# Kernel tuning notes

Hardware: AMD Instinct MI355X
Metric: run time of the kernel (lower is better)

The kernel has to match this reference:

```python
import jax, jax.numpy as jnp
import numpy as np

A_NUM = 9
C_NUM = 20


def generate_anchor(anc, grid):
    # anc: (A,2) w,h ; grid: (B,H,W,2) centers -> anchors (B,A,H,W,4)
    centers = grid[:, None]                      # (B,1,H,W,2)
    half = anc.reshape(1, -1, 1, 1, 2) * 0.5     # (1,A,1,1,2)
    return jnp.concatenate([centers - half, centers + half], axis=-1)


def iou_matrix(proposals, bboxes):
    # proposals: (B,A,H,W,4) -> (B,K,4); bboxes: (B,N,5)
    B = proposals.shape[0]
    p = proposals.reshape(B, -1, 4)[:, :, None, :]   # (B,K,1,4)
    bb = bboxes[:, None, :, :]                       # (B,1,N,5)
    s_p = (p[..., 2] - p[..., 0]) * (p[..., 3] - p[..., 1])
    s_b = (bb[..., 2] - bb[..., 0]) * (bb[..., 3] - bb[..., 1])
    ix1 = jnp.maximum(p[..., 0], bb[..., 0])
    iy1 = jnp.maximum(p[..., 1], bb[..., 1])
    ix2 = jnp.minimum(p[..., 2], bb[..., 2])
    iy2 = jnp.minimum(p[..., 3], bb[..., 3])
    s_i = jnp.clip(ix2 - ix1, 0.0) * jnp.clip(iy2 - iy1, 0.0)
    s_u = s_p + s_b - s_i
    iou = jnp.clip(s_i / (s_u + 1e-8), 0.0)
    invalid = (s_u <= 0) | (s_p <= 0) | (s_b <= 0) | (bb[..., 0] < 0)
    return jnp.where(invalid, 0.0, iou)              # (B,K,N)


def extract_anchor_data(anchor_data, idx):
    # anchor_data: (B,A,D,H,W) -> flat (B*A*H*W, D) -> gather
    B, A, D, H, W = anchor_data.shape
    flat = jnp.transpose(anchor_data, (0, 1, 3, 4, 2)).reshape(-1, D)
    return flat[idx]


def extract_class_scores(all_scores, idx, num_anchors):
    # all_scores: (B,C,H,W) -> (B,A,H,W,C) flat -> gather
    B, C, H, W = all_scores.shape
    s = jnp.transpose(all_scores, (0, 2, 3, 1))[:, None]          # (B,1,H,W,C)
    s = jnp.broadcast_to(s, (B, num_anchors, H, W, C)).reshape(-1, C)
    return s[idx]


def setup_inputs() -> dict:
    key = jax.random.key(0)
    ks = jax.random.split(key, 8)
    B, Cin, H, W = 32, 1280, 28, 28
    N, M = 64, 4096
    hid, out_ch = 128, 5 * A_NUM + C_NUM
    features = jax.random.normal(ks[0], (B, Cin, H, W), dtype=jnp.float32)
    # grid of feature-cell centers (GenerateGrid-style)
    xs = jnp.arange(W, dtype=jnp.float32) + 0.5
    ys = jnp.arange(H, dtype=jnp.float32) + 0.5
    gx, gy = jnp.meshgrid(xs, ys, indexing='xy')
    grid = jnp.broadcast_to(jnp.stack([gx, gy], axis=-1), (B, H, W, 2))
    anc = jnp.array([[1.0, 1], [2, 2], [3, 3], [4, 4], [5, 5], [2, 3], [3, 2], [3, 5], [5, 3]], dtype=jnp.float32)
    tl = jax.random.uniform(ks[1], (B, N, 2), minval=0.0, maxval=20.0)
    wh = jax.random.uniform(ks[2], (B, N, 2), minval=1.0, maxval=8.0)
    cls = jax.random.randint(ks[3], (B, N, 1), 0, C_NUM).astype(jnp.float32)
    bb = jnp.concatenate([tl, tl + wh, cls], axis=-1)
    valid = jax.random.uniform(ks[4], (B, N, 1)) > 0.25
    bboxes = jnp.where(valid, bb, -1.0)
    K = B * A_NUM * H * W
    pos_anchor_idx = jax.random.randint(ks[5], (M,), 0, K, dtype=jnp.int64 if jax.config.jax_enable_x64 else jnp.int32)
    neg_anchor_idx = jax.random.randint(ks[6], (M,), 0, K, dtype=pos_anchor_idx.dtype)
    W1 = jax.random.normal(ks[7], (hid, Cin), dtype=jnp.float32) * 0.02
    b1 = jnp.zeros((hid,), dtype=jnp.float32)
    W2 = jax.random.normal(jax.random.fold_in(key, 99), (out_ch, hid), dtype=jnp.float32) * 0.02
    b2 = jnp.zeros((out_ch,), dtype=jnp.float32)
    return {"features": features, "grid": grid, "anc": anc, "bboxes": bboxes,
            "pos_anchor_idx": pos_anchor_idx, "neg_anchor_idx": neg_anchor_idx,
            "W1": W1, "b1": b1, "W2": W2, "b2": b2}


def reference(features, grid, anc, bboxes, pos_anchor_idx, neg_anchor_idx, W1, b1, W2, b2):
    B, Cin, H, W = features.shape
    A, C = A_NUM, C_NUM
    # anchors + broadcast IoU matrix
    anchors = generate_anchor(anc, grid)                 # (B,A,H,W,4)
    iou_mat = iou_matrix(anchors, bboxes)                # (B,A*H*W,N)
    # prediction head: 1x1 conv -> (dropout eval: identity) -> leaky_relu -> 1x1 conv
    h = jnp.einsum('bchw,oc->bohw', features, W1) + b1[None, :, None, None]
    h = jax.nn.leaky_relu(h, negative_slope=0.01)
    out = jnp.einsum('bchw,oc->bohw', h, W2) + b2[None, :, None, None]  # (B,5A+C,H,W)
    anchor_raw = out[:, :5 * A].reshape(B, A, 5, H, W)
    conf_sq = jax.nn.sigmoid(anchor_raw[:, :, 0:1])      # (B,A,1,H,W)
    off_raw = anchor_raw[:, :, 1:]                       # (B,A,4,H,W)
    off_sq = jnp.concatenate([jax.nn.sigmoid(off_raw[:, :, :2]) - 0.5, off_raw[:, :, 2:]], axis=2)
    class_raw = out[:, 5 * A:]                           # (B,C,H,W)
    # training path: irregular gathers
    class_scores = extract_class_scores(class_raw, pos_anchor_idx, A)   # (M,C)
    offsets = extract_anchor_data(off_sq, pos_anchor_idx)               # (M,4)
    conf_pos = extract_anchor_data(conf_sq, pos_anchor_idx)             # (M,1)
    conf_neg = extract_anchor_data(conf_sq, neg_anchor_idx)             # (M,1)
    conf_scores = jnp.concatenate([conf_pos, conf_neg], axis=0)         # (2M,1)
    return conf_scores, offsets, class_scores, iou_mat
```

## Files before the change

### kernel.cpp

```cpp
#include <hip/hip_runtime.h>
#include <cstdint>

#define A_NUM 9
#define C_NUM 20
#define B_SZ 32
#define HW 784
#define P_NUM (A_NUM*HW)
#define NBOX 64
#define CIN 1280
#define HID 128
#define M_IDX 4096
#define KSPLIT 2
#define ASTR 40
#define PSTR ((size_t)B_SZ * HW * HID)
#define IOU_PB 64
#define TP_HW 196
#define TP_S 197

#define CONF_OFF 0
#define OFFS_OFF (2*M_IDX)
#define CLS_OFF  (OFFS_OFF + 4*M_IDX)
#define IOU_OFF  (CLS_OFF + C_NUM*M_IDX)

typedef short bf16x8 __attribute__((ext_vector_type(8)));
typedef float f32x4  __attribute__((ext_vector_type(4)));

__device__ __forceinline__ unsigned pack_bf16(float lo, float hi) {
  unsigned a = __builtin_bit_cast(unsigned, lo);
  unsigned b = __builtin_bit_cast(unsigned, hi);
  return ((a + 0x8000u) >> 16) | ((b + 0x8000u) & 0xffff0000u);
}

__global__ __launch_bounds__(256) void transpose_pack(
    const float* __restrict__ F, unsigned* __restrict__ Ft) {
  __shared__ unsigned T2[32 * TP_S];
  const int b = blockIdx.z;
  const int cc = blockIdx.y;
  const int hc = blockIdx.x;
  const int t = threadIdx.x;
  const int c0 = cc * 64, hw0 = hc * TP_HW;
  const float* Fb = F + ((size_t)b * CIN + c0) * HW + hw0;
  for (int i = 0; i < 7; i++) {
    int slot = t + 256 * i;
    if (slot < 1568) {
      int rp = slot / 49, ch = slot - rp * 49;
      const float* s0 = Fb + (size_t)(2 * rp) * HW + ch * 4;
      float4 lo4 = *(const float4*)s0;
      float4 hi4 = *(const float4*)(s0 + HW);
      unsigned* d = &T2[rp * TP_S + ch * 4];
      d[0] = pack_bf16(lo4.x, hi4.x);
      d[1] = pack_bf16(lo4.y, hi4.y);
      d[2] = pack_bf16(lo4.z, hi4.z);
      d[3] = pack_bf16(lo4.w, hi4.w);
    }
  }
  __syncthreads();
  unsigned* Fo = Ft + ((size_t)b * HW + hw0) * (CIN / 2) + c0 / 2;
  for (int i = 0; i < 13; i++) {
    int id = t + 256 * i;
    if (id < 3136) {
      int hw = id >> 4, ch = id & 15;
      uint2 v;
      v.x = T2[(2 * ch) * TP_S + hw];
      v.y = T2[(2 * ch + 1) * TP_S + hw];
      *(uint2*)&Fo[(size_t)hw * (CIN / 2) + ch * 2] = v;
    }
  }
}

__global__ __launch_bounds__(256) void prep_w1(const float* __restrict__ W1,
                                               uint4* __restrict__ W1f) {
  int id = blockIdx.x * 256 + threadIdx.x;
  int lane = id & 63;
  int ntile = (id >> 6) & 7;
  int ks = id >> 9;
  int lo = lane & 15, quad = lane >> 4;
  int n = ntile * 16 + lo;
  int k0 = ks * 32 + quad * 8;
  const float* src = W1 + n * CIN + k0;
  float4 x = *(const float4*)src;
  float4 y = *(const float4*)(src + 4);
  uint4 p;
  p.x = pack_bf16(x.x, x.y);
  p.y = pack_bf16(x.z, x.w);
  p.z = pack_bf16(y.x, y.y);
  p.w = pack_bf16(y.z, y.w);
  W1f[id] = p;
}

__global__ __launch_bounds__(256) void gemm1_mfma(
    const unsigned short* __restrict__ Ft, const unsigned short* __restrict__ W1f,
    float* __restrict__ Part) {
  __shared__ unsigned short Asm[2][64 * ASTR];

  const int b = blockIdx.y, z = blockIdx.z;
  const int m0 = blockIdx.x * 64;
  const int t = threadIdx.x;
  const int wave = t >> 6, lane = t & 63;
  const int quad = lane >> 4, lo = lane & 15;
  const int sm = t >> 2, kc = t & 3;
  const int gm = m0 + sm;
  const unsigned short* Fr =
      Ft + ((size_t)b * HW + (gm < HW ? gm : 0)) * CIN + z * 640;

  f32x4 acc[4][2];
#pragma unroll
  for (int i = 0; i < 4; i++)
#pragma unroll
    for (int j = 0; j < 2; j++) acc[i][j] = (f32x4){0.f, 0.f, 0.f, 0.f};

  uint4 va;
  uint4 vb[2][2];

  auto loadA = [&](int kk) { va = *(const uint4*)(Fr + kk * 32 + kc * 8); };
  auto loadB = [&](int kk, uint4* dst) {
    const unsigned short* g =
        W1f + (size_t)((((z * 20 + kk) * 8) + wave * 2) * 64 + lane) * 8;
    dst[0] = *(const uint4*)g;
    dst[1] = *(const uint4*)(g + 512);
  };
  auto stageA = [&](int buf) {
    *(uint4*)&Asm[buf][sm * ASTR + kc * 8] = va;
  };
  auto compute = [&](int buf, uint4* bv) {
    const unsigned short* Ab = &Asm[buf][lo * ASTR + quad * 8];
    bf16x8 af[4];
#pragma unroll
    for (int i = 0; i < 4; i++) af[i] = *(const bf16x8*)(Ab + i * 16 * ASTR);
    bf16x8 b0 = __builtin_bit_cast(bf16x8, bv[0]);
    bf16x8 b1 = __builtin_bit_cast(bf16x8, bv[1]);
#pragma unroll
    for (int i = 0; i < 4; i++) {
      acc[i][0] = __builtin_amdgcn_mfma_f32_16x16x32_bf16(af[i], b0, acc[i][0], 0, 0, 0);
      acc[i][1] = __builtin_amdgcn_mfma_f32_16x16x32_bf16(af[i], b1, acc[i][1], 0, 0, 0);
    }
  };

  loadA(0);
  loadB(0, vb[0]);
  stageA(0);
  __syncthreads();
  for (int kk = 0; kk < 20; kk++) {
    const int cur = kk & 1;
    if (kk + 1 < 20) {
      loadA(kk + 1);
      loadB(kk + 1, vb[cur ^ 1]);
    }
    compute(cur, vb[cur]);
    if (kk + 1 < 20) stageA(cur ^ 1);
    __syncthreads();
  }

  float* Pz = Part + ((size_t)(z * B_SZ + b) * HW) * HID;
#pragma unroll
  for (int i = 0; i < 4; i++) {
    const int mbase = m0 + i * 16 + quad * 4;
#pragma unroll
    for (int j = 0; j < 2; j++) {
      const int n = wave * 32 + j * 16 + lo;
#pragma unroll
      for (int r = 0; r < 4; r++) {
        const int mm = mbase + r;
        if (mm < HW) Pz[(size_t)mm * HID + n] = acc[i][j][r];
      }
    }
  }
}

__global__ __launch_bounds__(256) void iou_kernel(
    const float* __restrict__ grid, const float* __restrict__ anc,
    const float* __restrict__ bboxes, float* __restrict__ out) {
  __shared__ float sb[NBOX * 5];
  __shared__ float4 sp4[IOU_PB];
  const int b = blockIdx.y;
  const int p0 = blockIdx.x * IOU_PB;
  const int t = threadIdx.x;
  for (int i = t; i < NBOX * 5; i += 256) sb[i] = bboxes[b * NBOX * 5 + i];
  if (t < IOU_PB) {
    int p = p0 + t;
    float x1 = 0.f, y1 = 0.f, x2 = 0.f, y2 = 0.f;
    if (p < P_NUM) {
      int a = p / HW, hw = p - a * HW;
      float2 c = ((const float2*)grid)[b * HW + hw];
      float hx = anc[a * 2 + 0] * 0.5f, hy = anc[a * 2 + 1] * 0.5f;
      x1 = c.x - hx; y1 = c.y - hy; x2 = c.x + hx; y2 = c.y + hy;
    }
    sp4[t] = make_float4(x1, y1, x2, y2);
  }
  __syncthreads();
  const int nl = (t & 15) * 4;
  const int pi = t >> 4;
#pragma unroll
  for (int ip = 0; ip < 4; ip++) {
    const int pl = pi + 16 * ip;
    const int p = p0 + pl;
    const float4 pb = sp4[pl];
    const float spA = (pb.z - pb.x) * (pb.w - pb.y);
    float4 res;
#pragma unroll
    for (int jn = 0; jn < 4; jn++) {
      const int n = nl + jn;
      float bx1 = sb[n * 5 + 0], by1 = sb[n * 5 + 1];
      float bx2 = sb[n * 5 + 2], by2 = sb[n * 5 + 3];
      float s_b = (bx2 - bx1) * (by2 - by1);
      float ix1 = fmaxf(pb.x, bx1), iy1 = fmaxf(pb.y, by1);
      float ix2 = fminf(pb.z, bx2), iy2 = fminf(pb.w, by2);
      float si = fmaxf(ix2 - ix1, 0.f) * fmaxf(iy2 - iy1, 0.f);
      float su = spA + s_b - si;
      float iou = fmaxf(si / (su + 1e-8f), 0.f);
      bool invalid = (su <= 0.f) | (spA <= 0.f) | (s_b <= 0.f) | (bx1 < 0.f);
      float v = invalid ? 0.f : iou;
      if (jn == 0) res.x = v; else if (jn == 1) res.y = v;
      else if (jn == 2) res.z = v; else res.w = v;
    }
    if (p < P_NUM)
      *(float4*)&out[((size_t)(b * P_NUM + p)) * 64 + nl] = res;
  }
}

__global__ __launch_bounds__(256) void gather_kernel(
    const int* __restrict__ pos_idx, const int* __restrict__ neg_idx,
    const float* __restrict__ Part, const float* __restrict__ b1,
    const float* __restrict__ W2, const float* __restrict__ b2,
    float* __restrict__ out) {
  __shared__ float sh[4][HID];
  const int sub = threadIdx.x >> 6;
  const int l = threadIdx.x & 63;
  const int blk = blockIdx.x * 4 + sub;
  const bool pos = blk < M_IDX;
  const int idx = pos ? pos_idx[blk] : neg_idx[blk - M_IDX];
  const int b = idx / P_NUM;
  const int r = idx - b * P_NUM;
  const int a = r / HW;
  const int hw = r - a * HW;
  const float2* row = (const float2*)(Part + ((size_t)(b * HW + hw)) * HID) + l;
  float2 s0 = row[0];
  float2 s1 = row[PSTR / 2];
  float v0 = s0.x + s1.x + b1[2 * l];
  float v1 = s0.y + s1.y + b1[2 * l + 1];
  v0 = v0 > 0.f ? v0 : 0.01f * v0;
  v1 = v1 > 0.f ? v1 : 0.01f * v1;
  sh[sub][2 * l] = v0; sh[sub][2 * l + 1] = v1;
  __syncthreads();
  if (pos) {
    if (l < 25) {
      int o = (l < 5) ? (a * 5 + l) : (5 * A_NUM + (l - 5));
      const float* w = W2 + o * HID;
      float dot = b2[o];
#pragma unroll 8
      for (int k = 0; k < HID; k++) dot = fmaf(w[k], sh[sub][k], dot);
      if (l == 0) {
        out[CONF_OFF + blk] = 1.f / (1.f + expf(-dot));
      } else if (l < 3) {
        out[OFFS_OFF + blk * 4 + (l - 1)] = 1.f / (1.f + expf(-dot)) - 0.5f;
      } else if (l < 5) {
        out[OFFS_OFF + blk * 4 + (l - 1)] = dot;
      } else {
        out[CLS_OFF + blk * C_NUM + (l - 5)] = dot;
      }
    }
  } else {
    int o = a * 5;
    const float* w = W2 + o * HID;
    float part = fmaf(w[2 * l], v0, w[2 * l + 1] * v1);
#pragma unroll
    for (int off = 32; off > 0; off >>= 1) part += __shfl_down(part, off);
    if (l == 0) out[CONF_OFF + blk] = 1.f / (1.f + expf(-(b2[o] + part)));
  }
}

extern "C" void kernel_launch(void* const* d_in, const int* in_sizes, int n_in,
                              void* d_out, int out_size, void* d_ws, size_t ws_size,
                              hipStream_t stream) {
  const float* features = (const float*)d_in[0];
  const float* grid     = (const float*)d_in[1];
  const float* anc      = (const float*)d_in[2];
  const float* bboxes   = (const float*)d_in[3];
  const int*   pos_idx  = (const int*)d_in[4];
  const int*   neg_idx  = (const int*)d_in[5];
  const float* W1       = (const float*)d_in[6];
  const float* b1       = (const float*)d_in[7];
  const float* W2       = (const float*)d_in[8];
  const float* b2       = (const float*)d_in[9];
  float* out = (float*)d_out;

  uint4* W1f = (uint4*)d_ws;
  unsigned* Ft = (unsigned*)((char*)d_ws + 327680);
  float* Part = (float*)((char*)d_ws + 327680 + 64225280);

  hipLaunchKernelGGL(transpose_pack, dim3(4, 20, B_SZ), dim3(256), 0, stream,
                     features, Ft);
  hipLaunchKernelGGL(prep_w1, dim3(80), dim3(256), 0, stream, W1, W1f);
  hipLaunchKernelGGL(gemm1_mfma, dim3(13, B_SZ, KSPLIT), dim3(256), 0, stream,
                     (const unsigned short*)Ft, (const unsigned short*)W1f, Part);
  hipLaunchKernelGGL(iou_kernel, dim3((P_NUM + IOU_PB - 1) / IOU_PB, B_SZ),
                     dim3(256), 0, stream, grid, anc, bboxes, out + IOU_OFF);
  hipLaunchKernelGGL(gather_kernel, dim3(2 * M_IDX / 4), dim3(256),
                     0, stream, pos_idx, neg_idx, Part, b1, W2, b2, out);
}
```

Baseline: 276.3 us.

## Fuse first-layer GEMM with gather, computing hidden activations only for indexed anchors

Replaces the full-map split-K first-layer GEMM plus separate gather kernel with one kernel. It gathers feature rows for the positive and negative indices, runs the MFMA GEMM over the full K, applies bias and leaky ReLU into shared memory, and computes the second-layer dot products directly. This skips hidden-layer work for anchors that are never gathered and removes the fp32 partial-sum round trip through global memory. In exchange the GEMM runs on only 128 blocks with scattered row loads and a longer K loop per block.

```diff
diff --git a/kernel.cpp b/kernel.cpp
--- a/kernel.cpp
+++ b/kernel.cpp
@@ -10,9 +10,7 @@
 #define CIN 1280
 #define HID 128
 #define M_IDX 4096
-#define KSPLIT 2
 #define ASTR 40
-#define PSTR ((size_t)B_SZ * HW * HID)
 #define IOU_PB 64
 #define TP_HW 196
 #define TP_S 197
@@ -88,20 +86,30 @@
   W1f[id] = p;
 }
 
-__global__ __launch_bounds__(256) void gemm1_mfma(
+__global__ __launch_bounds__(256) void head_kernel(
+    const int* __restrict__ pos_idx, const int* __restrict__ neg_idx,
     const unsigned short* __restrict__ Ft, const unsigned short* __restrict__ W1f,
-    float* __restrict__ Part) {
+    const float* __restrict__ b1, const float* __restrict__ W2,
+    const float* __restrict__ b2, float* __restrict__ out) {
   __shared__ unsigned short Asm[2][64 * ASTR];
-
-  const int b = blockIdx.y, z = blockIdx.z;
-  const int m0 = blockIdx.x * 64;
+  __shared__ float hbuf[64][132];
+  __shared__ int sa[64];
+
   const int t = threadIdx.x;
   const int wave = t >> 6, lane = t & 63;
   const int quad = lane >> 4, lo = lane & 15;
+  const int s0 = blockIdx.x * 64;
+  const bool posb = s0 < M_IDX;
+
   const int sm = t >> 2, kc = t & 3;
-  const int gm = m0 + sm;
-  const unsigned short* Fr =
-      Ft + ((size_t)b * HW + (gm < HW ? gm : 0)) * CIN + z * 640;
+  const int gs = s0 + sm;
+  const int idx = posb ? pos_idx[gs] : neg_idx[gs - M_IDX];
+  const int b = idx / P_NUM;
+  const int r = idx - b * P_NUM;
+  const int a = r / HW;
+  const int hw = r - a * HW;
+  if (kc == 0) sa[sm] = a;
+  const unsigned short* Fr = Ft + ((size_t)(b * HW) + hw) * CIN;
 
   f32x4 acc[4][2];
 #pragma unroll
@@ -114,25 +122,22 @@
 
   auto loadA = [&](int kk) { va = *(const uint4*)(Fr + kk * 32 + kc * 8); };
   auto loadB = [&](int kk, uint4* dst) {
-    const unsigned short* g =
-        W1f + (size_t)((((z * 20 + kk) * 8) + wave * 2) * 64 + lane) * 8;
+    const unsigned short* g = W1f + (size_t)(((kk * 8) + wave * 2) * 64 + lane) * 8;
     dst[0] = *(const uint4*)g;
     dst[1] = *(const uint4*)(g + 512);
   };
-  auto stageA = [&](int buf) {
-    *(uint4*)&Asm[buf][sm * ASTR + kc * 8] = va;
-  };
+  auto stageA = [&](int buf) { *(uint4*)&Asm[buf][sm * ASTR + kc * 8] = va; };
   auto compute = [&](int buf, uint4* bv) {
     const unsigned short* Ab = &Asm[buf][lo * ASTR + quad * 8];
     bf16x8 af[4];
 #pragma unroll
     for (int i = 0; i < 4; i++) af[i] = *(const bf16x8*)(Ab + i * 16 * ASTR);
     bf16x8 b0 = __builtin_bit_cast(bf16x8, bv[0]);
-    bf16x8 b1 = __builtin_bit_cast(bf16x8, bv[1]);
+    bf16x8 b1v = __builtin_bit_cast(bf16x8, bv[1]);
 #pragma unroll
     for (int i = 0; i < 4; i++) {
       acc[i][0] = __builtin_amdgcn_mfma_f32_16x16x32_bf16(af[i], b0, acc[i][0], 0, 0, 0);
-      acc[i][1] = __builtin_amdgcn_mfma_f32_16x16x32_bf16(af[i], b1, acc[i][1], 0, 0, 0);
+      acc[i][1] = __builtin_amdgcn_mfma_f32_16x16x32_bf16(af[i], b1v, acc[i][1], 0, 0, 0);
     }
   };
 
@@ -140,29 +145,67 @@
   loadB(0, vb[0]);
   stageA(0);
   __syncthreads();
-  for (int kk = 0; kk < 20; kk++) {
+  for (int kk = 0; kk < 40; kk++) {
     const int cur = kk & 1;
-    if (kk + 1 < 20) {
+    if (kk + 1 < 40) {
       loadA(kk + 1);
       loadB(kk + 1, vb[cur ^ 1]);
     }
     compute(cur, vb[cur]);
-    if (kk + 1 < 20) stageA(cur ^ 1);
+    if (kk + 1 < 40) stageA(cur ^ 1);
     __syncthreads();
   }
 
-  float* Pz = Part + ((size_t)(z * B_SZ + b) * HW) * HID;
 #pragma unroll
   for (int i = 0; i < 4; i++) {
-    const int mbase = m0 + i * 16 + quad * 4;
+    const int mrow = i * 16 + quad * 4;
 #pragma unroll
     for (int j = 0; j < 2; j++) {
       const int n = wave * 32 + j * 16 + lo;
-#pragma unroll
-      for (int r = 0; r < 4; r++) {
-        const int mm = mbase + r;
-        if (mm < HW) Pz[(size_t)mm * HID + n] = acc[i][j][r];
+      const float bias = b1[n];
+#pragma unroll
+      for (int r2 = 0; r2 < 4; r2++) {
+        float v = acc[i][j][r2] + bias;
+        hbuf[mrow + r2][n] = v > 0.f ? v : 0.01f * v;
       }
+    }
+  }
+  __syncthreads();
+
+  for (int it = 0; it < 16; it++) {
+    const int sl = wave * 16 + it;
+    const int g = s0 + sl;
+    const int aa = sa[sl];
+    if (posb) {
+      if (lane < 25) {
+        const int o = (lane < 5) ? aa * 5 + lane : 5 * A_NUM + (lane - 5);
+        const float4* w4 = (const float4*)(W2 + o * HID);
+        const float4* h4 = (const float4*)hbuf[sl];
+        float dot = b2[o];
+#pragma unroll 8
+        for (int k = 0; k < 32; k++) {
+          float4 w = w4[k];
+          float4 h = h4[k];
+          dot = fmaf(w.x, h.x, fmaf(w.y, h.y, fmaf(w.z, h.z, fmaf(w.w, h.w, dot))));
+        }
+        if (lane == 0) {
+          out[CONF_OFF + g] = 1.f / (1.f + expf(-dot));
+        } else if (lane < 3) {
+          out[OFFS_OFF + g * 4 + (lane - 1)] = 1.f / (1.f + expf(-dot)) - 0.5f;
+        } else if (lane < 5) {
+          out[OFFS_OFF + g * 4 + (lane - 1)] = dot;
+        } else {
+          out[CLS_OFF + g * C_NUM + (lane - 5)] = dot;
+        }
+      }
+    } else {
+      const int o = aa * 5;
+      const float2 w2v = *(const float2*)&W2[o * HID + 2 * lane];
+      const float2 h2 = *(const float2*)&hbuf[sl][2 * lane];
+      float part = fmaf(w2v.x, h2.x, w2v.y * h2.y);
+#pragma unroll
+      for (int off = 32; off > 0; off >>= 1) part += __shfl_down(part, off);
+      if (lane == 0) out[CONF_OFF + g] = 1.f / (1.f + expf(-(b2[o] + part)));
     }
   }
 }
@@ -218,57 +261,6 @@
   }
 }
 
-__global__ __launch_bounds__(256) void gather_kernel(
-    const int* __restrict__ pos_idx, const int* __restrict__ neg_idx,
-    const float* __restrict__ Part, const float* __restrict__ b1,
-    const float* __restrict__ W2, const float* __restrict__ b2,
-    float* __restrict__ out) {
-  __shared__ float sh[4][HID];
-  const int sub = threadIdx.x >> 6;
-  const int l = threadIdx.x & 63;
-  const int blk = blockIdx.x * 4 + sub;
-  const bool pos = blk < M_IDX;
-  const int idx = pos ? pos_idx[blk] : neg_idx[blk - M_IDX];
-  const int b = idx / P_NUM;
-  const int r = idx - b * P_NUM;
-  const int a = r / HW;
-  const int hw = r - a * HW;
-  const float2* row = (const float2*)(Part + ((size_t)(b * HW + hw)) * HID) + l;
-  float2 s0 = row[0];
-  float2 s1 = row[PSTR / 2];
-  float v0 = s0.x + s1.x + b1[2 * l];
-  float v1 = s0.y + s1.y + b1[2 * l + 1];
-  v0 = v0 > 0.f ? v0 : 0.01f * v0;
-  v1 = v1 > 0.f ? v1 : 0.01f * v1;
-  sh[sub][2 * l] = v0; sh[sub][2 * l + 1] = v1;
-  __syncthreads();
-  if (pos) {
-    if (l < 25) {
-      int o = (l < 5) ? (a * 5 + l) : (5 * A_NUM + (l - 5));
-      const float* w = W2 + o * HID;
-      float dot = b2[o];
-#pragma unroll 8
-      for (int k = 0; k < HID; k++) dot = fmaf(w[k], sh[sub][k], dot);
-      if (l == 0) {
-        out[CONF_OFF + blk] = 1.f / (1.f + expf(-dot));
-      } else if (l < 3) {
-        out[OFFS_OFF + blk * 4 + (l - 1)] = 1.f / (1.f + expf(-dot)) - 0.5f;
-      } else if (l < 5) {
-        out[OFFS_OFF + blk * 4 + (l - 1)] = dot;
-      } else {
-        out[CLS_OFF + blk * C_NUM + (l - 5)] = dot;
-      }
-    }
-  } else {
-    int o = a * 5;
-    const float* w = W2 + o * HID;
-    float part = fmaf(w[2 * l], v0, w[2 * l + 1] * v1);
-#pragma unroll
-    for (int off = 32; off > 0; off >>= 1) part += __shfl_down(part, off);
-    if (l == 0) out[CONF_OFF + blk] = 1.f / (1.f + expf(-(b2[o] + part)));
-  }
-}
-
 extern "C" void kernel_launch(void* const* d_in, const int* in_sizes, int n_in,
                               void* d_out, int out_size, void* d_ws, size_t ws_size,
                               hipStream_t stream) {
@@ -286,15 +278,13 @@
 
   uint4* W1f = (uint4*)d_ws;
   unsigned* Ft = (unsigned*)((char*)d_ws + 327680);
-  float* Part = (float*)((char*)d_ws + 327680 + 64225280);
 
   hipLaunchKernelGGL(transpose_pack, dim3(4, 20, B_SZ), dim3(256), 0, stream,
                      features, Ft);
   hipLaunchKernelGGL(prep_w1, dim3(80), dim3(256), 0, stream, W1, W1f);
-  hipLaunchKernelGGL(gemm1_mfma, dim3(13, B_SZ, KSPLIT), dim3(256), 0, stream,
-                     (const unsigned short*)Ft, (const unsigned short*)W1f, Part);
+  hipLaunchKernelGGL(head_kernel, dim3(2 * M_IDX / 64), dim3(256), 0, stream,
+                     pos_idx, neg_idx, (const unsigned short*)Ft,
+                     (const unsigned short*)W1f, b1, W2, b2, out);
   hipLaunchKernelGGL(iou_kernel, dim3((P_NUM + IOU_PB - 1) / IOU_PB, B_SZ),
                      dim3(256), 0, stream, grid, anc, bboxes, out + IOU_OFF);
-  hipLaunchKernelGGL(gather_kernel, dim3(2 * M_IDX / 4), dim3(256),
-                     0, stream, pos_idx, neg_idx, Part, b1, W2, b2, out);
-}
+}
```

Result: slower. 294.8 us (+6.7%).
